# Optimization experiments

Measured on AMD Instinct MI355X. Metric: run time of the kernel, lower is better.

The kernel has to match this reference:

```python
import jax, jax.numpy as jnp
import numpy as np
from math import factorial

LMAX = 4
N_COEFF = (LMAX + 1) ** 2      # 25 real spherical-harmonic coefficients
N_RADII = 300                  # distance_bins
N_NODES = 512
FEAT = 128
RES_BETA, RES_ALPHA = 180, 360
DIST_STEP = 0.05


def _sh_basis(lmax, y, alpha):
    """Real spherical harmonics evaluated on a (beta, alpha) product grid.
    y = cos(beta) quadrature nodes. Returns [res_beta, res_alpha, (lmax+1)^2]."""
    B, A = len(y), len(alpha)
    P = np.zeros((lmax + 1, lmax + 1, B))
    P[0, 0] = 1.0
    s = np.sqrt(np.clip(1.0 - y * y, 0.0, None))
    for m in range(1, lmax + 1):
        P[m, m] = -(2 * m - 1) * s * P[m - 1, m - 1]
    for m in range(lmax):
        P[m + 1, m] = (2 * m + 1) * y * P[m, m]
    for m in range(lmax + 1):
        for l in range(m + 2, lmax + 1):
            P[l, m] = ((2 * l - 1) * y * P[l - 1, m] - (l + m - 1) * P[l - 2, m]) / (l - m)
    cols = []
    for l in range(lmax + 1):
        for m in range(-l, l + 1):
            am = abs(m)
            Nlm = np.sqrt((2 * l + 1) / (4 * np.pi) * factorial(l - am) / factorial(l + am))
            if m == 0:
                col = Nlm * P[l, 0][:, None] * np.ones((1, A))
            elif m > 0:
                col = np.sqrt(2.0) * Nlm * P[l, m][:, None] * np.cos(m * alpha)[None, :]
            else:
                col = np.sqrt(2.0) * Nlm * P[l, am][:, None] * np.sin(am * alpha)[None, :]
            cols.append(col)
    return np.stack(cols, axis=-1).astype(np.float32)


def setup_inputs() -> dict:
    key = jax.random.key(0)
    ks = jax.random.split(key, 14)

    def lin(k, a, b):
        return jax.random.normal(k, (a, b), jnp.float32) / np.float32(np.sqrt(a))

    x = jax.random.normal(ks[0], (N_NODES, FEAT), jnp.float32)
    fd = [FEAT, 128, 128, 64, 16, 2]
    td = [FEAT, 128, 128, 128, 128, 128, 6]
    fW = [lin(ks[1 + i], fd[i], fd[i + 1]) for i in range(5)]
    tW = [lin(ks[6 + i], td[i], td[i + 1]) for i in range(6)]
    pos_w = lin(ks[12], 2 * FEAT, N_RADII * N_COEFF)
    type_emb = jax.random.normal(ks[13], (5, FEAT), jnp.float32)

    y_np, w_np = np.polynomial.legendre.leggauss(RES_BETA)
    alpha_np = np.linspace(0.0, 2.0 * np.pi, RES_ALPHA, endpoint=False)
    basis = jnp.asarray(_sh_basis(LMAX, y_np, alpha_np))          # [B, A, C]
    qw = jnp.asarray(w_np / 2.0, jnp.float32)                     # gausslegendre / 2
    y_grid = jnp.asarray(y_np, jnp.float32)
    alpha_grid = jnp.asarray(alpha_np, jnp.float32)

    return {
        "x": x,
        "focus_w1": fW[0], "focus_w2": fW[1], "focus_w3": fW[2], "focus_w4": fW[3], "focus_w5": fW[4],
        "type_w1": tW[0], "type_w2": tW[1], "type_w3": tW[2], "type_w4": tW[3], "type_w5": tW[4], "type_w6": tW[5],
        "pos_w": pos_w, "type_emb": type_emb,
        "basis": basis, "qw": qw, "y_grid": y_grid, "alpha_grid": alpha_grid,
        "res_beta": RES_BETA, "res_alpha": RES_ALPHA,
    }


def reference(x, focus_w1, focus_w2, focus_w3, focus_w4, focus_w5,
              type_w1, type_w2, type_w3, type_w4, type_w5, type_w6,
              pos_w, type_emb, basis, qw, y_grid, alpha_grid,
              res_beta, res_alpha):
    n_nodes = x.shape[0]

    # --- focus MLP (relu), per-node logits; STOP logit 0 appended ---
    h = x
    for W in (focus_w1, focus_w2, focus_w3, focus_w4):
        h = jax.nn.relu(h @ W)
    focus_scores = (h @ focus_w5)[:, 0]                             # [n_nodes]
    focus_probs = jax.nn.softmax(jnp.concatenate([focus_scores, jnp.zeros((1,), x.dtype)]))
    focus = jnp.minimum(jnp.argmax(focus_probs), n_nodes - 1)

    # --- type MLP (softplus) on the focus node's features ---
    feat_f = x[focus]                                               # [128]
    th = feat_f
    for W in (type_w1, type_w2, type_w3, type_w4, type_w5):
        th = jax.nn.softplus(th @ W)
    type_dist = jax.nn.softmax(th @ type_w6)                        # [6]
    type_idx = jnp.minimum(jnp.argmax(type_dist), 4)

    # --- position head: SH coefficients per radial shell ---
    pos_in = jnp.concatenate([feat_f, type_emb[type_idx]])          # [256]
    coeffs = (pos_in @ pos_w).reshape(N_RADII, N_COEFF)             # [R, C]

    # to_s2grid: log-density on the sphere for every radial shell
    f = jnp.einsum('rc,bac->rba', coeffs, basis)                    # [R, B, A]
    log_meas = jnp.log(qw)[:, None] + jnp.log(2.0 * jnp.pi / res_alpha)  # [B, 1]

    # radial distribution: integral of exp(f) over the sphere, per shell
    log_radial = jax.nn.logsumexp(f + log_meas[None], axis=(1, 2))  # [R]
    radial_probs = jax.nn.softmax(log_radial)

    key = jax.random.key(42)
    k_r, k_a = jax.random.split(key)
    r_idx = jax.random.categorical(k_r, log_radial)

    # angular distribution at the sampled radius, normalized on S2
    fr = f[r_idx]                                                   # [B, A]
    logZr = jax.nn.logsumexp(fr + log_meas)
    angular_dist = jnp.exp(fr - logZr)                              # [B, A]

    joint_log = (fr + log_meas - logZr).reshape(-1)
    idx = jax.random.categorical(k_a, joint_log)
    y_i = idx // res_alpha
    a_i = idx % res_alpha

    radius_pred = (r_idx.astype(jnp.float32) + 1.0) * DIST_STEP
    return (type_dist, radial_probs, angular_dist, radius_pred, y_grid[y_i], alpha_grid[a_i])
```

## Files before the change

kernel.cpp:

```cpp
#include <hip/hip_runtime.h>
#include <math.h>
#include <stdint.h>

#define NNODES 512
#define FEAT   128
#define NR     300
#define NC     25
#define NB     180
#define NA     360
#define RSPLIT 4
#define BCHUNK (NB / RSPLIT)
#define O_TYPE   0
#define O_RAD    6
#define O_ANG    306
#define O_RADIUS 65106
#define O_Y      65107
#define O_ALPHA  65108

#define WS_KEYS   0
#define WS_TYPEI  5
#define WS_DEAD   8
#define WS_AKEY   16
#define WS_ACNT   18
#define WS_SCORES 320
#define WS_Q      1664
#define WS_CXF    6176
#define WS_CEM    13696
#define WS_LRP    51200

#define G1_MLP   64
#define G1_PREP  18
#define G1_PFT   21
#define G1_CEM   118
#define G1_TOTAL (G1_MLP + G1_PREP + G1_PFT + G1_CEM)

__constant__ int c_m_of_c[25] = {0,-1,0,1,-2,-1,0,1,2,-3,-2,-1,0,1,2,3,-4,-3,-2,-1,0,1,2,3,4};
__constant__ int c_h_cnt[9] = {5,4,3,2,1,4,3,2,1};
__constant__ int c_h_idx[9][5] = {
  {0,2,6,12,20},
  {3,7,13,21,0},
  {8,14,22,0,0},
  {15,23,0,0,0},
  {24,0,0,0,0},
  {1,5,11,19,0},
  {4,10,18,0,0},
  {9,17,0,0,0},
  {16,0,0,0,0}};

__device__ __forceinline__ void tf2x32(uint32_t k0, uint32_t k1, uint32_t x0, uint32_t x1,
                                       uint32_t& o0, uint32_t& o1) {
  uint32_t ks2 = k0 ^ k1 ^ 0x1BD11BDAu;
#define TF_RND(r) { x0 += x1; x1 = (x1 << r) | (x1 >> (32 - r)); x1 ^= x0; }
  x0 += k0; x1 += k1;
  TF_RND(13) TF_RND(15) TF_RND(26) TF_RND(6)
  x0 += k1; x1 += ks2 + 1u;
  TF_RND(17) TF_RND(29) TF_RND(16) TF_RND(24)
  x0 += ks2; x1 += k0 + 2u;
  TF_RND(13) TF_RND(15) TF_RND(26) TF_RND(6)
  x0 += k0; x1 += k1 + 3u;
  TF_RND(17) TF_RND(29) TF_RND(16) TF_RND(24)
  x0 += k1; x1 += ks2 + 4u;
  TF_RND(13) TF_RND(15) TF_RND(26) TF_RND(6)
  x0 += ks2; x1 += k0 + 5u;
#undef TF_RND
  o0 = x0; o1 = x1;
}

__device__ __forceinline__ float gumbel32(uint32_t k0, uint32_t k1, uint32_t lo) {
  uint32_t o0, o1; tf2x32(k0, k1, 0u, lo, o0, o1);
  uint32_t bits = o0 ^ o1;
  float u = __uint_as_float((bits >> 9) | 0x3f800000u) - 1.0f;
  u = fmaxf(u, 1.1754944e-38f);
  return -logf(-logf(u));
}

__device__ __forceinline__ float softplusf(float s) {
  return fmaxf(s, 0.f) + log1pf(expf(-fabsf(s)));
}

__global__ __launch_bounds__(256) void k_front(const float* __restrict__ x,
    const float* __restrict__ w1, const float* __restrict__ w2, const float* __restrict__ w3,
    const float* __restrict__ w4, const float* __restrict__ w5,
    const float* __restrict__ basis, const float* __restrict__ alpha_grid,
    const float* __restrict__ tw1, const float* __restrict__ tw2, const float* __restrict__ tw3,
    const float* __restrict__ tw4, const float* __restrict__ tw5, const float* __restrict__ tw6,
    const float* __restrict__ pos_w, const float* __restrict__ type_emb,
    float* __restrict__ wsf) {
  __shared__ float A[8][128];
  __shared__ float B[8][128];
  int bx = blockIdx.x, t = threadIdx.x;

  if (bx < G1_MLP) {
    int base = bx * 8;
    for (int i = t; i < 8 * 128; i += 256) A[i >> 7][i & 127] = x[(base + (i >> 7)) * FEAT + (i & 127)];
    __syncthreads();
    int j = t & 127, h = t >> 7;
    {
      float a0 = 0, a1 = 0, a2 = 0, a3 = 0;
#pragma unroll 8
      for (int k = 0; k < 128; k++) {
        float wv = w1[k * 128 + j];
        a0 += A[h * 4 + 0][k] * wv; a1 += A[h * 4 + 1][k] * wv;
        a2 += A[h * 4 + 2][k] * wv; a3 += A[h * 4 + 3][k] * wv;
      }
      __syncthreads();
      B[h * 4 + 0][j] = fmaxf(a0, 0.f); B[h * 4 + 1][j] = fmaxf(a1, 0.f);
      B[h * 4 + 2][j] = fmaxf(a2, 0.f); B[h * 4 + 3][j] = fmaxf(a3, 0.f);
      __syncthreads();
    }
    {
      float a0 = 0, a1 = 0, a2 = 0, a3 = 0;
#pragma unroll 8
      for (int k = 0; k < 128; k++) {
        float wv = w2[k * 128 + j];
        a0 += B[h * 4 + 0][k] * wv; a1 += B[h * 4 + 1][k] * wv;
        a2 += B[h * 4 + 2][k] * wv; a3 += B[h * 4 + 3][k] * wv;
      }
      __syncthreads();
      A[h * 4 + 0][j] = fmaxf(a0, 0.f); A[h * 4 + 1][j] = fmaxf(a1, 0.f);
      A[h * 4 + 2][j] = fmaxf(a2, 0.f); A[h * 4 + 3][j] = fmaxf(a3, 0.f);
      __syncthreads();
    }
    {
      int j3 = t & 63, g = t >> 6;
      float a0 = 0, a1 = 0;
#pragma unroll 8
      for (int k = 0; k < 128; k++) {
        float wv = w3[k * 64 + j3];
        a0 += A[g * 2 + 0][k] * wv; a1 += A[g * 2 + 1][k] * wv;
      }
      __syncthreads();
      B[g * 2 + 0][j3] = fmaxf(a0, 0.f); B[g * 2 + 1][j3] = fmaxf(a1, 0.f);
      __syncthreads();
    }
    {
      int j4 = t & 15, g4 = t >> 4;
      if (g4 < 8) {
        float a0 = 0;
#pragma unroll
        for (int k = 0; k < 64; k++) a0 += B[g4][k] * w4[k * 16 + j4];
        A[g4][j4] = fmaxf(a0, 0.f);
      }
      __syncthreads();
    }
    if (t < 8) {
      float a0 = 0;
#pragma unroll
      for (int k = 0; k < 16; k++) a0 += A[t][k] * w5[k * 2 + 0];
      wsf[WS_SCORES + base + t] = a0;
    }
  } else if (bx < G1_MLP + G1_PREP) {
    int p = (bx - G1_MLP) * 256 + t;
    if (bx == G1_MLP && t == 0) {
      uint32_t* wu = (uint32_t*)wsf;
      uint32_t o0, o1;
      tf2x32(0u, 42u, 0u, 0u, o0, o1); wu[WS_KEYS + 0] = o0; wu[WS_KEYS + 1] = o1;
      tf2x32(0u, 42u, 0u, 1u, o0, o1); wu[WS_KEYS + 2] = o0; wu[WS_KEYS + 3] = o1;
    }
    if (p < NB * NC) {
      int b = p / NC, c = p % NC;
      int m = c_m_of_c[c];
      float q;
      if (m >= 0) {
        q = basis[(b * NA + 0) * NC + c];
      } else {
        float a10 = alpha_grid[10];
        q = basis[(b * NA + 10) * NC + c] / sinf((float)(-m) * a10);
      }
      wsf[WS_Q + p] = q;
    }
  } else if (bx < G1_MLP + G1_PREP + G1_PFT) {
    const float4* mats[5] = {(const float4*)tw1, (const float4*)tw2, (const float4*)tw3,
                             (const float4*)tw4, (const float4*)tw5};
    int lid = (bx - (G1_MLP + G1_PREP)) * 256 + t;
    float acc = 0.f;
    for (int vi = lid; vi < 20672; vi += G1_PFT * 256) {
      int mi = vi >> 12;
      float4 v;
      if (mi < 5) v = mats[mi][vi & 4095];
      else        v = ((const float4*)tw6)[vi - 20480];
      acc += v.x + v.y + v.z + v.w;
    }
    if (acc == -1.2345678e30f) wsf[WS_DEAD] = acc;
  } else {
    __shared__ float es[5 * 128];
    __shared__ float part[5][4][64];
    int cb = bx - (G1_MLP + G1_PREP + G1_PFT);
    for (int i = t; i < 640; i += 256) es[i] = type_emb[i];
    __syncthreads();
    int oL = t & 63, kc = t >> 6;
    int o = cb * 64 + oL;
    float e0 = 0, e1 = 0, e2 = 0, e3 = 0, e4 = 0;
    if (o < NR * NC) {
#pragma unroll 8
      for (int k8 = 0; k8 < 32; k8++) {
        int k = kc * 32 + k8;
        float wv = pos_w[(128 + k) * (NR * NC) + o];
        e0 += es[k] * wv;        e1 += es[128 + k] * wv;
        e2 += es[256 + k] * wv;  e3 += es[384 + k] * wv;
        e4 += es[512 + k] * wv;
      }
    }
    part[0][kc][oL] = e0; part[1][kc][oL] = e1; part[2][kc][oL] = e2;
    part[3][kc][oL] = e3; part[4][kc][oL] = e4;
    __syncthreads();
    if (t < 64) {
      int oo = cb * 64 + t;
      if (oo < NR * NC) {
#pragma unroll
        for (int ti = 0; ti < 5; ti++) {
          float s = part[ti][0][t] + part[ti][1][t] + part[ti][2][t] + part[ti][3][t];
          wsf[WS_CEM + ti * (NR * NC) + oo] = s;
        }
      }
    }
  }
}

__global__ __launch_bounds__(1024) void k_mid(const float* __restrict__ x,
    const float* __restrict__ w1, const float* __restrict__ w2, const float* __restrict__ w3,
    const float* __restrict__ w4, const float* __restrict__ w5, const float* __restrict__ w6,
    const float* __restrict__ pos_w,
    float* __restrict__ out, float* __restrict__ wsf) {
  __shared__ float wrv[16]; __shared__ int wri[16];
  __shared__ int f_sh;
  int t = threadIdx.x;
  int lane = t & 63, wid = t >> 6;
  float bv = -INFINITY; int bi = 1 << 30;
  if (t < NNODES + 1) { bv = (t < NNODES) ? wsf[WS_SCORES + t] : 0.f; bi = t; }
  for (int off = 32; off; off >>= 1) {
    float v2 = __shfl_down(bv, off); int i2 = __shfl_down(bi, off);
    if (v2 > bv || (v2 == bv && i2 < bi)) { bv = v2; bi = i2; }
  }
  if (lane == 0) { wrv[wid] = bv; wri[wid] = bi; }
  __syncthreads();
  if (t == 0) {
    float v0 = wrv[0]; int i0 = wri[0];
    for (int w = 1; w < 16; w++)
      if (wrv[w] > v0 || (wrv[w] == v0 && wri[w] < i0)) { v0 = wrv[w]; i0 = wri[w]; }
    f_sh = (i0 < NNODES - 1) ? i0 : (NNODES - 1);
  }
  __syncthreads();
  int focus = f_sh;

  if (blockIdx.x == 0) {
    __shared__ float src[128];
    __shared__ float partial[8][128];
    __shared__ float lg[6];
    if (t < 128) src[t] = x[focus * FEAT + t];
    __syncthreads();
    const float* Ws[5] = {w1, w2, w3, w4, w5};
#pragma unroll
    for (int L = 0; L < 5; L++) {
      const float* W = Ws[L];
      int j = t & 127, kc = t >> 7;
      float acc = 0.f;
#pragma unroll
      for (int k = 0; k < 16; k++) acc += src[kc * 16 + k] * W[(kc * 16 + k) * 128 + j];
      partial[kc][j] = acc;
      __syncthreads();
      if (t < 128) {
        float s = 0.f;
#pragma unroll
        for (int q = 0; q < 8; q++) s += partial[q][t];
        src[t] = softplusf(s);
      }
      __syncthreads();
    }
    float prod = 0.f;
    if (t < 768) { int o = t >> 7, j = t & 127; prod = src[j] * w6[j * 6 + o]; }
    for (int off = 32; off; off >>= 1) prod += __shfl_down(prod, off);
    if (t < 768 && lane == 0) wrv[wid] = prod;
    __syncthreads();
    if (t == 0) {
      float lg[6];
      for (int o = 0; o < 6; o++) lg[o] = wrv[2 * o] + wrv[2 * o + 1];
      float M = lg[0]; int am = 0;
      for (int i = 1; i < 6; i++) if (lg[i] > M) { M = lg[i]; am = i; }
      float e[6], S = 0.f;
      for (int i = 0; i < 6; i++) { e[i] = expf(lg[i] - M); S += e[i]; }
      for (int i = 0; i < 6; i++) out[O_TYPE + i] = e[i] / S;
      ((int*)wsf)[WS_TYPEI] = (am < 4) ? am : 4;
    }
  } else {
    __shared__ float xf[128];
    __shared__ float px[16][64];
    if (t < 128) xf[t] = x[focus * FEAT + t];
    __syncthreads();
    int oL = t & 63, kc = t >> 6;
    int o = (blockIdx.x - 1) * 64 + oL;
    float ax = 0.f;
    if (o < NR * NC) {
#pragma unroll
      for (int k8 = 0; k8 < 8; k8++) {
        int k = kc * 8 + k8;
        ax += xf[k] * pos_w[k * (NR * NC) + o];
      }
    }
    px[kc][oL] = ax;
    __syncthreads();
    if (t < 64) {
      int oo = (blockIdx.x - 1) * 64 + t;
      if (oo < NR * NC) {
        float s = 0.f;
#pragma unroll
        for (int q = 0; q < 16; q++) s += px[q][t];
        wsf[WS_CXF + oo] = s;
      }
    }
  }
}

__global__ __launch_bounds__(384) void k_radial_lse(const float* __restrict__ qw,
    const float* __restrict__ alpha_grid, float* __restrict__ wsf) {
  __shared__ float4 Hs4[BCHUNK * 3];
  __shared__ float cs[NC];
  __shared__ float wred[6];
  int bx = blockIdx.x;
  int r = bx >> 2, s = bx & 3;
  int b0 = s * BCHUNK;
  int t = threadIdx.x;
  float* Hs = (float*)Hs4;
  if (bx == 0 && t == 0) {
    *(unsigned long long*)(wsf + WS_AKEY) = 0ULL;
    *(unsigned int*)(wsf + WS_ACNT) = 0u;
  }
  int ti = ((const int*)wsf)[WS_TYPEI];
  if (t < NC) cs[t] = wsf[WS_CXF + r * NC + t] + wsf[WS_CEM + ti * (NR * NC) + r * NC + t];
  __syncthreads();
  const float LOGM = -4.0482054576f;
  for (int p = t; p < BCHUNK * 9; p += 384) {
    int b = p / 9, jj = p % 9;
    int bg = b0 + b;
    int n = c_h_cnt[jj];
    float acc = 0.f;
    for (int q = 0; q < n; q++) { int c = c_h_idx[jj][q]; acc += cs[c] * wsf[WS_Q + bg * NC + c]; }
    if (jj == 0) acc += logf(qw[bg]) + LOGM;
    Hs[b * 12 + jj] = acc;
  }
  __syncthreads();
  float c1 = 0, c2 = 0, c3 = 0, c4 = 0, s1 = 0, s2 = 0, s3 = 0, s4 = 0;
  bool act = t < NA;
  if (act) {
    float al = alpha_grid[t];
    sincosf(al, &s1, &c1);
    sincosf(2.f * al, &s2, &c2);
    sincosf(3.f * al, &s3, &c3);
    sincosf(4.f * al, &s4, &c4);
  }
  float acc = 0.f;
#pragma unroll 5
  for (int b = 0; b < BCHUNK; b++) {
    float4 h0 = Hs4[b * 3 + 0], h1 = Hs4[b * 3 + 1], h2 = Hs4[b * 3 + 2];
    float f = h0.x + h0.y * c1 + h0.z * c2 + h0.w * c3 + h1.x * c4
            + h1.y * s1 + h1.z * s2 + h1.w * s3 + h2.x * s4;
    acc += act ? __expf(f) : 0.f;
  }
  for (int off = 32; off; off >>= 1) acc += __shfl_down(acc, off);
  int wid = t >> 6, lane = t & 63;
  if (lane == 0) wred[wid] = acc;
  __syncthreads();
  if (t == 0) {
    float ss = 0.f;
    for (int w = 0; w < 6; w++) ss += wred[w];
    wsf[WS_LRP + bx] = ss;
  }
}

__global__ __launch_bounds__(384) void k_ang(const float* __restrict__ qw,
    const float* __restrict__ alpha_grid, const float* __restrict__ y_grid,
    float* __restrict__ out, float* __restrict__ wsf) {
  __shared__ float wred[6]; __shared__ int wri[6];
  __shared__ float fss[NR];
  __shared__ float cs[NC];
  __shared__ float hsh[12];
  __shared__ float S_sh; __shared__ int r_sh;
  int b = blockIdx.x, t = threadIdx.x;
  int lane = t & 63, wid = t >> 6;
  const uint32_t* wu = (const uint32_t*)wsf;
  uint32_t kr0 = wu[WS_KEYS + 0], kr1 = wu[WS_KEYS + 1];
  uint32_t ka0 = wu[WS_KEYS + 2], ka1 = wu[WS_KEYS + 3];
  int ti = ((const int*)wsf)[WS_TYPEI];

  float sv = 0.f, lr = -INFINITY;
  if (t < NR) {
    sv = wsf[WS_LRP + 4 * t] + wsf[WS_LRP + 4 * t + 1]
       + wsf[WS_LRP + 4 * t + 2] + wsf[WS_LRP + 4 * t + 3];
    fss[t] = sv;
    lr = logf(sv);
  }
  float ss = sv;
  for (int off = 32; off; off >>= 1) ss += __shfl_down(ss, off);
  if (lane == 0) wred[wid] = ss;
  __syncthreads();
  if (t == 0) {
    float S = 0.f;
    for (int w = 0; w < 6; w++) S += wred[w];
    S_sh = S;
  }
  __syncthreads();
  if (b == 0 && t < NR) out[O_RAD + t] = sv / S_sh;
  float v = (t < NR) ? lr + gumbel32(kr0, kr1, (uint32_t)t) : -INFINITY;
  int bi = (t < NR) ? t : (1 << 30);
  for (int off = 32; off; off >>= 1) {
    float v2 = __shfl_down(v, off); int i2 = __shfl_down(bi, off);
    if (v2 > v || (v2 == v && i2 < bi)) { v = v2; bi = i2; }
  }
  __syncthreads();
  if (lane == 0) { wred[wid] = v; wri[wid] = bi; }
  __syncthreads();
  if (t == 0) {
    float v0 = wred[0]; int i0 = wri[0];
    for (int w = 1; w < 6; w++)
      if (wred[w] > v0 || (wred[w] == v0 && wri[w] < i0)) { v0 = wred[w]; i0 = wri[w]; }
    r_sh = i0;
    if (b == 0) out[O_RADIUS] = (float)(i0 + 1) * 0.05f;
  }
  __syncthreads();
  int r = r_sh;
  float invZ = 1.0f / fss[r];

  if (t < NC) cs[t] = wsf[WS_CXF + r * NC + t] + wsf[WS_CEM + ti * (NR * NC) + r * NC + t];
  __syncthreads();
  if (t < 9) {
    int n = c_h_cnt[t];
    float acc = 0.f;
    for (int q = 0; q < n; q++) { int c = c_h_idx[t][q]; acc += cs[c] * wsf[WS_Q + b * NC + c]; }
    hsh[t] = acc;
  }
  __syncthreads();
  const float MEAS = 0.01745329252f;
  float elm = qw[b] * MEAS;
  float lm = logf(elm);
  float va = -INFINITY; int idx = (t < NA) ? b * NA + t : (1 << 30);
  if (t < NA) {
    float al = alpha_grid[t];
    float s1, c1, s2, c2, s3, c3, s4, c4;
    sincosf(al, &s1, &c1); sincosf(2.f * al, &s2, &c2);
    sincosf(3.f * al, &s3, &c3); sincosf(4.f * al, &s4, &c4);
    float f = hsh[0] + hsh[1] * c1 + hsh[2] * c2 + hsh[3] * c3 + hsh[4] * c4
            + hsh[5] * s1 + hsh[6] * s2 + hsh[7] * s3 + hsh[8] * s4;
    out[O_ANG + idx] = __expf(f) * invZ;
    va = f + lm + gumbel32(ka0, ka1, (uint32_t)idx);
  }
  for (int off = 32; off; off >>= 1) {
    float v2 = __shfl_down(va, off); int i2 = __shfl_down(idx, off);
    if (v2 > va || (v2 == va && i2 < idx)) { va = v2; idx = i2; }
  }
  __syncthreads();
  if (lane == 0) { wred[wid] = va; wri[wid] = idx; }
  __syncthreads();
  if (t == 0) {
    float v0 = wred[0]; int i0 = wri[0];
    for (int w = 1; w < 6; w++)
      if (wred[w] > v0 || (wred[w] == v0 && wri[w] < i0)) { v0 = wred[w]; i0 = wri[w]; }
    uint32_t u = __float_as_uint(v0);
    uint32_t ordv = (u & 0x80000000u) ? ~u : (u | 0x80000000u);
    unsigned long long key = ((unsigned long long)ordv << 32)
                           | (unsigned long long)(0xFFFFFFFFu - (uint32_t)i0);
    atomicMax((unsigned long long*)(wsf + WS_AKEY), key);
    __threadfence();
    unsigned int old = atomicAdd((unsigned int*)(wsf + WS_ACNT), 1u);
    if (old == NB - 1) {
      __threadfence();
      unsigned long long kk = atomicMax((unsigned long long*)(wsf + WS_AKEY), 0ULL);
      uint32_t gidx = 0xFFFFFFFFu - (uint32_t)(kk & 0xFFFFFFFFull);
      int yi = (int)(gidx / NA), ai = (int)(gidx % NA);
      out[O_Y] = y_grid[yi];
      out[O_ALPHA] = alpha_grid[ai];
    }
  }
}

extern "C" void kernel_launch(void* const* d_in, const int* in_sizes, int n_in,
                              void* d_out, int out_size, void* d_ws, size_t ws_size,
                              hipStream_t stream) {
  const float* x          = (const float*)d_in[0];
  const float* fw1        = (const float*)d_in[1];
  const float* fw2        = (const float*)d_in[2];
  const float* fw3        = (const float*)d_in[3];
  const float* fw4        = (const float*)d_in[4];
  const float* fw5        = (const float*)d_in[5];
  const float* tw1        = (const float*)d_in[6];
  const float* tw2        = (const float*)d_in[7];
  const float* tw3        = (const float*)d_in[8];
  const float* tw4        = (const float*)d_in[9];
  const float* tw5        = (const float*)d_in[10];
  const float* tw6        = (const float*)d_in[11];
  const float* pos_w      = (const float*)d_in[12];
  const float* type_emb   = (const float*)d_in[13];
  const float* basis      = (const float*)d_in[14];
  const float* qw         = (const float*)d_in[15];
  const float* y_grid     = (const float*)d_in[16];
  const float* alpha_grid = (const float*)d_in[17];
  (void)in_sizes; (void)n_in; (void)out_size; (void)ws_size;
  float* out = (float*)d_out;
  float* wsf = (float*)d_ws;

  k_front<<<G1_TOTAL, 256, 0, stream>>>(x, fw1, fw2, fw3, fw4, fw5, basis, alpha_grid,
                                        tw1, tw2, tw3, tw4, tw5, tw6, pos_w, type_emb, wsf);
  k_mid<<<1 + (NR * NC + 63) / 64, 1024, 0, stream>>>(x, tw1, tw2, tw3, tw4, tw5, tw6,
                                                      pos_w, out, wsf);
  k_radial_lse<<<NR * RSPLIT, 384, 0, stream>>>(qw, alpha_grid, wsf);
  k_ang<<<NB, 384, 0, stream>>>(qw, alpha_grid, y_grid, out, wsf);
}
```

Baseline: 56.35 us.

## Eliminate k_mid launch by speculatively computing type MLP for all nodes

Removes the middle kernel that waited on the focus argmax. The type MLP is now evaluated for every node in k_front, and pos_w's x-half is transposed into workspace, so both steps run before the focus is known. Each downstream block then recomputes the focus argmax and the 25 needed coefficients for its radius from the transposed rows. This saves one launch and one serialization point, at the cost of about 512x more type-MLP work and redundant per-block argmax and dot products. It also drops the prefetch-only blocks.

```diff
diff --git a/kernel.cpp b/kernel.cpp
--- a/kernel.cpp
+++ b/kernel.cpp
@@ -18,21 +18,21 @@
 #define O_ALPHA  65108
 
 #define WS_KEYS   0
-#define WS_TYPEI  5
-#define WS_DEAD   8
 #define WS_AKEY   16
 #define WS_ACNT   18
 #define WS_SCORES 320
-#define WS_Q      1664
-#define WS_CXF    6176
-#define WS_CEM    13696
-#define WS_LRP    51200
-
-#define G1_MLP   64
-#define G1_PREP  18
-#define G1_PFT   21
-#define G1_CEM   118
-#define G1_TOTAL (G1_MLP + G1_PREP + G1_PFT + G1_CEM)
+#define WS_TLOG   840
+#define WS_Q      4000
+#define WS_CEM    8512
+#define WS_LRP    46016
+#define WS_PWT    47232
+
+#define R_SC  64
+#define R_TY  128
+#define R_PR  146
+#define R_CE  264
+#define R_TR  323
+#define G1_TOTAL R_TR
 
 __constant__ int c_m_of_c[25] = {0,-1,0,1,-2,-1,0,1,2,-3,-2,-1,0,1,2,3,-4,-3,-2,-1,0,1,2,3,4};
 __constant__ int c_h_cnt[9] = {5,4,3,2,1,4,3,2,1};
@@ -78,6 +78,51 @@
   return fmaxf(s, 0.f) + log1pf(expf(-fabsf(s)));
 }
 
+__device__ __forceinline__ int focus_argmax384(const float* __restrict__ wsf,
+                                               float* swv, int* swi, int t) {
+  int lane = t & 63, wid = t >> 6;
+  float bv = (t < NNODES) ? wsf[WS_SCORES + t] : ((t == NNODES) ? 0.f : -INFINITY);
+  int bi = (t <= NNODES) ? t : (1 << 30);
+  int i2 = t + 384;
+  if (i2 <= NNODES) {
+    float v2 = (i2 < NNODES) ? wsf[WS_SCORES + i2] : 0.f;
+    if (v2 > bv) { bv = v2; bi = i2; }
+  }
+  for (int off = 32; off; off >>= 1) {
+    float v2 = __shfl_down(bv, off); int j2 = __shfl_down(bi, off);
+    if (v2 > bv || (v2 == bv && j2 < bi)) { bv = v2; bi = j2; }
+  }
+  if (lane == 0) { swv[wid] = bv; swi[wid] = bi; }
+  __syncthreads();
+  float v0 = swv[0]; int i0 = swi[0];
+  for (int w = 1; w < 6; w++)
+    if (swv[w] > v0 || (swv[w] == v0 && swi[w] < i0)) { v0 = swv[w]; i0 = swi[w]; }
+  __syncthreads();
+  return (i0 < NNODES - 1) ? i0 : (NNODES - 1);
+}
+
+__device__ __forceinline__ void cs_for_r(const float* __restrict__ pwt,
+                                         const float* __restrict__ wsf,
+                                         const float* xf, float* part, float* cs,
+                                         int r, int ti, int t) {
+  if (t < 375) {
+    int c = t / 15, kk = t % 15;
+    int kend = kk * 9 + 9; if (kend > 128) kend = 128;
+    float acc = 0.f;
+    const float* row = pwt + (size_t)(r * NC + c) * 128;
+    for (int k = kk * 9; k < kend; k++) acc += xf[k] * row[k];
+    part[c * 15 + kk] = acc;
+  }
+  __syncthreads();
+  if (t < NC) {
+    float a = 0.f;
+#pragma unroll
+    for (int kk = 0; kk < 15; kk++) a += part[t * 15 + kk];
+    cs[t] = a + wsf[WS_CEM + ti * (NR * NC) + r * NC + t];
+  }
+  __syncthreads();
+}
+
 __global__ __launch_bounds__(256) void k_front(const float* __restrict__ x,
     const float* __restrict__ w1, const float* __restrict__ w2, const float* __restrict__ w3,
     const float* __restrict__ w4, const float* __restrict__ w5,
@@ -86,11 +131,12 @@
     const float* __restrict__ tw4, const float* __restrict__ tw5, const float* __restrict__ tw6,
     const float* __restrict__ pos_w, const float* __restrict__ type_emb,
     float* __restrict__ wsf) {
-  __shared__ float A[8][128];
-  __shared__ float B[8][128];
+  __shared__ float SM[8256];
   int bx = blockIdx.x, t = threadIdx.x;
 
-  if (bx < G1_MLP) {
+  if (bx < R_SC) {
+    float (*A)[128] = (float(*)[128])SM;
+    float (*B)[128] = (float(*)[128])(SM + 1024);
     int base = bx * 8;
     for (int i = t; i < 8 * 128; i += 256) A[i >> 7][i & 127] = x[(base + (i >> 7)) * FEAT + (i & 127)];
     __syncthreads();
@@ -149,9 +195,51 @@
       for (int k = 0; k < 16; k++) a0 += A[t][k] * w5[k * 2 + 0];
       wsf[WS_SCORES + base + t] = a0;
     }
-  } else if (bx < G1_MLP + G1_PREP) {
-    int p = (bx - G1_MLP) * 256 + t;
-    if (bx == G1_MLP && t == 0) {
+  } else if (bx < R_TY) {
+    float* Abuf = SM;
+    float* Bbuf = SM + 1024;
+    float* P    = SM + 2048;
+    int base = (bx - R_SC) * 8;
+    for (int i = t; i < 1024; i += 256) Abuf[i] = x[(base + (i >> 7)) * FEAT + (i & 127)];
+    __syncthreads();
+    const float* Ws[5] = {tw1, tw2, tw3, tw4, tw5};
+    float* src = Abuf; float* dst = Bbuf;
+#pragma unroll
+    for (int L = 0; L < 5; L++) {
+      const float* W = Ws[L];
+      int j = t & 127, ks = t >> 7;
+      float a0 = 0, a1 = 0, a2 = 0, a3 = 0, a4 = 0, a5 = 0, a6 = 0, a7 = 0;
+#pragma unroll 8
+      for (int k0 = 0; k0 < 64; k0++) {
+        int k = ks * 64 + k0;
+        float wv = W[k * 128 + j];
+        a0 += src[0 * 128 + k] * wv; a1 += src[1 * 128 + k] * wv;
+        a2 += src[2 * 128 + k] * wv; a3 += src[3 * 128 + k] * wv;
+        a4 += src[4 * 128 + k] * wv; a5 += src[5 * 128 + k] * wv;
+        a6 += src[6 * 128 + k] * wv; a7 += src[7 * 128 + k] * wv;
+      }
+      float* Pk = P + ks * 1024;
+      Pk[0 * 128 + j] = a0; Pk[1 * 128 + j] = a1; Pk[2 * 128 + j] = a2; Pk[3 * 128 + j] = a3;
+      Pk[4 * 128 + j] = a4; Pk[5 * 128 + j] = a5; Pk[6 * 128 + j] = a6; Pk[7 * 128 + j] = a7;
+      __syncthreads();
+      int half = t >> 7;
+#pragma unroll
+      for (int q = 0; q < 4; q++) {
+        int n = half * 4 + q;
+        dst[n * 128 + j] = softplusf(P[n * 128 + j] + P[1024 + n * 128 + j]);
+      }
+      __syncthreads();
+      float* tmp = src; src = dst; dst = tmp;
+    }
+    if (t < 48) {
+      int n = t / 6, o = t % 6;
+      float a = 0.f;
+      for (int j = 0; j < 128; j++) a += src[n * 128 + j] * tw6[j * 6 + o];
+      wsf[WS_TLOG + (base + n) * 6 + o] = a;
+    }
+  } else if (bx < R_PR) {
+    int p = (bx - R_TY) * 256 + t;
+    if (bx == R_TY && t == 0) {
       uint32_t* wu = (uint32_t*)wsf;
       uint32_t o0, o1;
       tf2x32(0u, 42u, 0u, 0u, o0, o1); wu[WS_KEYS + 0] = o0; wu[WS_KEYS + 1] = o1;
@@ -169,23 +257,10 @@
       }
       wsf[WS_Q + p] = q;
     }
-  } else if (bx < G1_MLP + G1_PREP + G1_PFT) {
-    const float4* mats[5] = {(const float4*)tw1, (const float4*)tw2, (const float4*)tw3,
-                             (const float4*)tw4, (const float4*)tw5};
-    int lid = (bx - (G1_MLP + G1_PREP)) * 256 + t;
-    float acc = 0.f;
-    for (int vi = lid; vi < 20672; vi += G1_PFT * 256) {
-      int mi = vi >> 12;
-      float4 v;
-      if (mi < 5) v = mats[mi][vi & 4095];
-      else        v = ((const float4*)tw6)[vi - 20480];
-      acc += v.x + v.y + v.z + v.w;
-    }
-    if (acc == -1.2345678e30f) wsf[WS_DEAD] = acc;
-  } else {
-    __shared__ float es[5 * 128];
-    __shared__ float part[5][4][64];
-    int cb = bx - (G1_MLP + G1_PREP + G1_PFT);
+  } else if (bx < R_CE) {
+    float* es = SM;
+    float* part = SM + 640;
+    int cb = bx - R_PR;
     for (int i = t; i < 640; i += 256) es[i] = type_emb[i];
     __syncthreads();
     int oL = t & 63, kc = t >> 6;
@@ -201,133 +276,76 @@
         e4 += es[512 + k] * wv;
       }
     }
-    part[0][kc][oL] = e0; part[1][kc][oL] = e1; part[2][kc][oL] = e2;
-    part[3][kc][oL] = e3; part[4][kc][oL] = e4;
+    part[0 * 256 + kc * 64 + oL] = e0; part[1 * 256 + kc * 64 + oL] = e1;
+    part[2 * 256 + kc * 64 + oL] = e2; part[3 * 256 + kc * 64 + oL] = e3;
+    part[4 * 256 + kc * 64 + oL] = e4;
     __syncthreads();
     if (t < 64) {
       int oo = cb * 64 + t;
       if (oo < NR * NC) {
 #pragma unroll
         for (int ti = 0; ti < 5; ti++) {
-          float s = part[ti][0][t] + part[ti][1][t] + part[ti][2][t] + part[ti][3][t];
+          float s = part[ti * 256 + 0 * 64 + t] + part[ti * 256 + 1 * 64 + t]
+                  + part[ti * 256 + 2 * 64 + t] + part[ti * 256 + 3 * 64 + t];
           wsf[WS_CEM + ti * (NR * NC) + oo] = s;
         }
       }
     }
-  }
-}
-
-__global__ __launch_bounds__(1024) void k_mid(const float* __restrict__ x,
-    const float* __restrict__ w1, const float* __restrict__ w2, const float* __restrict__ w3,
-    const float* __restrict__ w4, const float* __restrict__ w5, const float* __restrict__ w6,
-    const float* __restrict__ pos_w,
+  } else {
+    float (*tile)[129] = (float(*)[129])SM;
+    float* pwt = wsf + WS_PWT;
+    int cb = bx - R_CE;
+    int o0 = cb * 128;
+#pragma unroll
+    for (int h = 0; h < 2; h++) {
+      int kb = h * 64;
+      __syncthreads();
+      int col = t & 127, rbase = t >> 7;
+      for (int rep = 0; rep < 32; rep++) {
+        int row = rbase + rep * 2;
+        tile[row][col] = (o0 + col < NR * NC) ? pos_w[(kb + row) * (NR * NC) + o0 + col] : 0.f;
+      }
+      __syncthreads();
+      int kk = t & 63, obase = t >> 6;
+      for (int rep = 0; rep < 32; rep++) {
+        int op = obase + rep * 4;
+        if (o0 + op < NR * NC) pwt[(size_t)(o0 + op) * 128 + kb + kk] = tile[kk][op];
+      }
+    }
+  }
+}
+
+__global__ __launch_bounds__(384) void k_lse(const float* __restrict__ x,
+    const float* __restrict__ qw, const float* __restrict__ alpha_grid,
     float* __restrict__ out, float* __restrict__ wsf) {
-  __shared__ float wrv[16]; __shared__ int wri[16];
-  __shared__ int f_sh;
-  int t = threadIdx.x;
-  int lane = t & 63, wid = t >> 6;
-  float bv = -INFINITY; int bi = 1 << 30;
-  if (t < NNODES + 1) { bv = (t < NNODES) ? wsf[WS_SCORES + t] : 0.f; bi = t; }
-  for (int off = 32; off; off >>= 1) {
-    float v2 = __shfl_down(bv, off); int i2 = __shfl_down(bi, off);
-    if (v2 > bv || (v2 == bv && i2 < bi)) { bv = v2; bi = i2; }
-  }
-  if (lane == 0) { wrv[wid] = bv; wri[wid] = bi; }
-  __syncthreads();
+  __shared__ float xf[128];
+  __shared__ float part[375];
+  __shared__ float cs[NC];
+  __shared__ float4 Hs4[BCHUNK * 3];
+  __shared__ float wred[6]; __shared__ int wri[6];
+  __shared__ int ti_sh;
+  int bx = blockIdx.x, t = threadIdx.x;
+  int r = bx >> 2, s = bx & 3, b0 = s * BCHUNK;
+  float* Hs = (float*)Hs4;
+
+  int focus = focus_argmax384(wsf, wred, wri, t);
+  if (t < 128) xf[t] = x[focus * FEAT + t];
   if (t == 0) {
-    float v0 = wrv[0]; int i0 = wri[0];
-    for (int w = 1; w < 16; w++)
-      if (wrv[w] > v0 || (wrv[w] == v0 && wri[w] < i0)) { v0 = wrv[w]; i0 = wri[w]; }
-    f_sh = (i0 < NNODES - 1) ? i0 : (NNODES - 1);
-  }
-  __syncthreads();
-  int focus = f_sh;
-
-  if (blockIdx.x == 0) {
-    __shared__ float src[128];
-    __shared__ float partial[8][128];
-    __shared__ float lg[6];
-    if (t < 128) src[t] = x[focus * FEAT + t];
-    __syncthreads();
-    const float* Ws[5] = {w1, w2, w3, w4, w5};
-#pragma unroll
-    for (int L = 0; L < 5; L++) {
-      const float* W = Ws[L];
-      int j = t & 127, kc = t >> 7;
-      float acc = 0.f;
-#pragma unroll
-      for (int k = 0; k < 16; k++) acc += src[kc * 16 + k] * W[(kc * 16 + k) * 128 + j];
-      partial[kc][j] = acc;
-      __syncthreads();
-      if (t < 128) {
-        float s = 0.f;
-#pragma unroll
-        for (int q = 0; q < 8; q++) s += partial[q][t];
-        src[t] = softplusf(s);
-      }
-      __syncthreads();
-    }
-    float prod = 0.f;
-    if (t < 768) { int o = t >> 7, j = t & 127; prod = src[j] * w6[j * 6 + o]; }
-    for (int off = 32; off; off >>= 1) prod += __shfl_down(prod, off);
-    if (t < 768 && lane == 0) wrv[wid] = prod;
-    __syncthreads();
-    if (t == 0) {
-      float lg[6];
-      for (int o = 0; o < 6; o++) lg[o] = wrv[2 * o] + wrv[2 * o + 1];
-      float M = lg[0]; int am = 0;
-      for (int i = 1; i < 6; i++) if (lg[i] > M) { M = lg[i]; am = i; }
+    const float* tl = wsf + WS_TLOG + focus * 6;
+    float M = tl[0]; int am = 0;
+    for (int i = 1; i < 6; i++) if (tl[i] > M) { M = tl[i]; am = i; }
+    ti_sh = (am < 4) ? am : 4;
+    if (bx == 0) {
       float e[6], S = 0.f;
-      for (int i = 0; i < 6; i++) { e[i] = expf(lg[i] - M); S += e[i]; }
+      for (int i = 0; i < 6; i++) { e[i] = expf(tl[i] - M); S += e[i]; }
       for (int i = 0; i < 6; i++) out[O_TYPE + i] = e[i] / S;
-      ((int*)wsf)[WS_TYPEI] = (am < 4) ? am : 4;
-    }
-  } else {
-    __shared__ float xf[128];
-    __shared__ float px[16][64];
-    if (t < 128) xf[t] = x[focus * FEAT + t];
-    __syncthreads();
-    int oL = t & 63, kc = t >> 6;
-    int o = (blockIdx.x - 1) * 64 + oL;
-    float ax = 0.f;
-    if (o < NR * NC) {
-#pragma unroll
-      for (int k8 = 0; k8 < 8; k8++) {
-        int k = kc * 8 + k8;
-        ax += xf[k] * pos_w[k * (NR * NC) + o];
-      }
-    }
-    px[kc][oL] = ax;
-    __syncthreads();
-    if (t < 64) {
-      int oo = (blockIdx.x - 1) * 64 + t;
-      if (oo < NR * NC) {
-        float s = 0.f;
-#pragma unroll
-        for (int q = 0; q < 16; q++) s += px[q][t];
-        wsf[WS_CXF + oo] = s;
-      }
-    }
-  }
-}
-
-__global__ __launch_bounds__(384) void k_radial_lse(const float* __restrict__ qw,
-    const float* __restrict__ alpha_grid, float* __restrict__ wsf) {
-  __shared__ float4 Hs4[BCHUNK * 3];
-  __shared__ float cs[NC];
-  __shared__ float wred[6];
-  int bx = blockIdx.x;
-  int r = bx >> 2, s = bx & 3;
-  int b0 = s * BCHUNK;
-  int t = threadIdx.x;
-  float* Hs = (float*)Hs4;
-  if (bx == 0 && t == 0) {
-    *(unsigned long long*)(wsf + WS_AKEY) = 0ULL;
-    *(unsigned int*)(wsf + WS_ACNT) = 0u;
-  }
-  int ti = ((const int*)wsf)[WS_TYPEI];
-  if (t < NC) cs[t] = wsf[WS_CXF + r * NC + t] + wsf[WS_CEM + ti * (NR * NC) + r * NC + t];
-  __syncthreads();
+      *(unsigned long long*)(wsf + WS_AKEY) = 0ULL;
+      *(unsigned int*)(wsf + WS_ACNT) = 0u;
+    }
+  }
+  __syncthreads();
+  cs_for_r(wsf + WS_PWT, wsf, xf, part, cs, r, ti_sh, t);
+
   const float LOGM = -4.0482054576f;
   for (int p = t; p < BCHUNK * 9; p += 384) {
     int b = p / 9, jj = p % 9;
@@ -358,6 +376,7 @@
   }
   for (int off = 32; off; off >>= 1) acc += __shfl_down(acc, off);
   int wid = t >> 6, lane = t & 63;
+  __syncthreads();
   if (lane == 0) wred[wid] = acc;
   __syncthreads();
   if (t == 0) {
@@ -367,20 +386,33 @@
   }
 }
 
-__global__ __launch_bounds__(384) void k_ang(const float* __restrict__ qw,
-    const float* __restrict__ alpha_grid, const float* __restrict__ y_grid,
+__global__ __launch_bounds__(384) void k_ang(const float* __restrict__ x,
+    const float* __restrict__ qw, const float* __restrict__ alpha_grid,
+    const float* __restrict__ y_grid,
     float* __restrict__ out, float* __restrict__ wsf) {
-  __shared__ float wred[6]; __shared__ int wri[6];
-  __shared__ float fss[NR];
+  __shared__ float xf[128];
+  __shared__ float part[375];
   __shared__ float cs[NC];
   __shared__ float hsh[12];
-  __shared__ float S_sh; __shared__ int r_sh;
+  __shared__ float fss[NR];
+  __shared__ float wred[6]; __shared__ int wri[6];
+  __shared__ float S_sh; __shared__ int r_sh, ti_sh;
   int b = blockIdx.x, t = threadIdx.x;
   int lane = t & 63, wid = t >> 6;
   const uint32_t* wu = (const uint32_t*)wsf;
   uint32_t kr0 = wu[WS_KEYS + 0], kr1 = wu[WS_KEYS + 1];
   uint32_t ka0 = wu[WS_KEYS + 2], ka1 = wu[WS_KEYS + 3];
-  int ti = ((const int*)wsf)[WS_TYPEI];
+
+  int focus = focus_argmax384(wsf, wred, wri, t);
+  if (t < 128) xf[t] = x[focus * FEAT + t];
+  if (t == 0) {
+    const float* tl = wsf + WS_TLOG + focus * 6;
+    float M = tl[0]; int am = 0;
+    for (int i = 1; i < 6; i++) if (tl[i] > M) { M = tl[i]; am = i; }
+    ti_sh = (am < 4) ? am : 4;
+  }
+  __syncthreads();
+  int ti = ti_sh;
 
   float sv = 0.f, lr = -INFINITY;
   if (t < NR) {
@@ -420,8 +452,7 @@
   int r = r_sh;
   float invZ = 1.0f / fss[r];
 
-  if (t < NC) cs[t] = wsf[WS_CXF + r * NC + t] + wsf[WS_CEM + ti * (NR * NC) + r * NC + t];
-  __syncthreads();
+  cs_for_r(wsf + WS_PWT, wsf, xf, part, cs, r, ti, t);
   if (t < 9) {
     int n = c_h_cnt[t];
     float acc = 0.f;
@@ -499,8 +530,6 @@
 
   k_front<<<G1_TOTAL, 256, 0, stream>>>(x, fw1, fw2, fw3, fw4, fw5, basis, alpha_grid,
                                         tw1, tw2, tw3, tw4, tw5, tw6, pos_w, type_emb, wsf);
-  k_mid<<<1 + (NR * NC + 63) / 64, 1024, 0, stream>>>(x, tw1, tw2, tw3, tw4, tw5, tw6,
-                                                      pos_w, out, wsf);
-  k_radial_lse<<<NR * RSPLIT, 384, 0, stream>>>(qw, alpha_grid, wsf);
-  k_ang<<<NB, 384, 0, stream>>>(qw, alpha_grid, y_grid, out, wsf);
-}
+  k_lse<<<NR * RSPLIT, 384, 0, stream>>>(x, qw, alpha_grid, out, wsf);
+  k_ang<<<NB, 384, 0, stream>>>(x, qw, alpha_grid, y_grid, out, wsf);
+}
```

New measurement: 124.2 us. 2.2x slower.
